# Kernel optimization log

Hardware: AMD Instinct MI355X
Metric: run time of the kernel (lower is better)

## Reference

```python
import jax, jax.numpy as jnp
import numpy as np

IN_FEATURES = 4096
OUT_FEATURES = 11008
GROUP_SIZE = 128
N_HIGH = 1024   # int(0.25*4096)//8*8
N_LOW = 3072    # (4096-1024)//8*8
M_TOKENS = 64


def unpack_6bit(packed, original_k):
    # packed: [K*3//4, N] uint8 values stored as int32
    _, N = packed.shape
    p = packed.reshape(original_k // 4, 3, N)
    b0, b1, b2 = p[:, 0], p[:, 1], p[:, 2]
    v0 = b0 & 63
    v1 = ((b0 >> 6) & 3) | ((b1 & 15) << 2)
    v2 = ((b1 >> 4) & 15) | ((b2 & 3) << 4)
    v3 = (b2 >> 2) & 63
    return jnp.stack([v0, v1, v2, v3], axis=1).reshape(original_k, N)


def unpack_5bit(packed, original_k):
    # packed: [K*5//8, N]
    _, N = packed.shape
    p = packed.reshape(original_k // 8, 5, N)
    b = [p[:, i] for i in range(5)]
    v0 = b[0] & 31
    v1 = ((b[0] >> 5) & 7) | ((b[1] & 3) << 3)
    v2 = (b[1] >> 2) & 31
    v3 = ((b[1] >> 7) & 1) | ((b[2] & 15) << 1)
    v4 = ((b[2] >> 4) & 15) | ((b[3] & 1) << 4)
    v5 = (b[3] >> 1) & 31
    v6 = ((b[3] >> 6) & 3) | ((b[4] & 7) << 2)
    v7 = (b[4] >> 3) & 31
    return jnp.stack([v0, v1, v2, v3, v4, v5, v6, v7], axis=1).reshape(original_k, N)


def dequant_region(W_q, scales, half_range):
    # W_q: [K, N] ints in [0, 2*half_range]; scales: [num_groups, N]
    K, N = W_q.shape
    G = scales.shape[0]
    Wg = (W_q.astype(jnp.float32) - float(half_range)).reshape(G, GROUP_SIZE, N)
    return (Wg * scales[:, None, :]).reshape(K, N)


def setup_inputs() -> dict:
    key = jax.random.key(0)
    ks = jax.random.split(key, 7)
    x = jax.random.normal(ks[0], (M_TOKENS, IN_FEATURES), dtype=jnp.float32)
    W_high_packed = jax.random.randint(ks[1], (N_HIGH * 3 // 4, OUT_FEATURES), 0, 256, dtype=jnp.int32)
    W_low_packed = jax.random.randint(ks[2], (N_LOW * 5 // 8, OUT_FEATURES), 0, 256, dtype=jnp.int32)
    scales_high = jax.random.uniform(ks[3], (N_HIGH // GROUP_SIZE, OUT_FEATURES), dtype=jnp.float32) * 0.02 + 1e-4
    scales_low = jax.random.uniform(ks[4], (N_LOW // GROUP_SIZE, OUT_FEATURES), dtype=jnp.float32) * 0.02 + 1e-4
    col_indices = jax.random.permutation(ks[5], IN_FEATURES).astype(jnp.int32)
    bias = jax.random.normal(ks[6], (OUT_FEATURES,), dtype=jnp.float32) * 0.02
    return {"x": x, "W_high_packed": W_high_packed, "W_low_packed": W_low_packed,
            "scales_high": scales_high, "scales_low": scales_low,
            "col_indices": col_indices, "bias": bias}


def reference(x, W_high_packed, W_low_packed, scales_high, scales_low, col_indices, bias):
    # Unpack mixed 6-bit / 5-bit weights and group-dequantize.
    Wq_high = unpack_6bit(W_high_packed, N_HIGH)          # [1024, N], 0..63
    Wq_low = unpack_5bit(W_low_packed, N_LOW)             # [3072, N], 0..31
    W_high = dequant_region(Wq_high, scales_high, 31)     # 6-bit half_range = 31
    W_low = dequant_region(Wq_low, scales_low, 15)        # 5-bit half_range = 15
    # Column-sensitivity reorder of activations, then split high/low regions.
    x_perm = x[:, col_indices]                            # [M, K]
    x_high = x_perm[:, :N_HIGH]
    x_low = x_perm[:, N_HIGH:N_HIGH + N_LOW]
    out = x_high @ W_high + x_low @ W_low + bias          # [M, N]
    return out
```

## Files before the change

### kernel.cpp

```cpp
#include <hip/hip_runtime.h>


#define NFEAT 11008
#define KTOT  4096

#define C2SIZE 45088768u

typedef _Float16     half8 __attribute__((ext_vector_type(8)));
typedef float        f32x4 __attribute__((ext_vector_type(4)));
typedef unsigned int u32x2 __attribute__((ext_vector_type(2)));
typedef unsigned int u32x4 __attribute__((ext_vector_type(4)));

#define GLOAD16(g, l) __builtin_amdgcn_global_load_lds(                         \
    (const __attribute__((address_space(1))) unsigned int*)(g),                 \
    (__attribute__((address_space(3))) unsigned int*)(l), 16, 0, 0)

#define DEQ8(w, s, mo, bf) do {                                                 \
    bf[0] = (_Float16)fmaf((float)((w)[0]         & 255u), (s), (mo));          \
    bf[1] = (_Float16)fmaf((float)(((w)[0] >>  8) & 255u), (s), (mo));          \
    bf[2] = (_Float16)fmaf((float)(((w)[0] >> 16) & 255u), (s), (mo));          \
    bf[3] = (_Float16)fmaf((float)( (w)[0] >> 24        ), (s), (mo));          \
    bf[4] = (_Float16)fmaf((float)((w)[1]         & 255u), (s), (mo));          \
    bf[5] = (_Float16)fmaf((float)(((w)[1] >>  8) & 255u), (s), (mo));          \
    bf[6] = (_Float16)fmaf((float)(((w)[1] >> 16) & 255u), (s), (mo));          \
    bf[7] = (_Float16)fmaf((float)( (w)[1] >> 24        ), (s), (mo));          \
} while (0)

__global__ __launch_bounds__(256) void prep_xfrag(const float* __restrict__ x,
                                                  const int* __restrict__ col,
                                                  _Float16* __restrict__ xfrag) {
    int idx = blockIdx.x * 256 + threadIdx.x;
    int j  = idx & 7;
    int l  = (idx >> 3) & 63;
    int mt = (idx >> 9) & 3;
    int s  = idx >> 11;
    int k  = s * 32 + ((l >> 4) << 3) + j;
    int m  = mt * 16 + (l & 15);
    xfrag[idx] = (_Float16)x[m * KTOT + col[k]];
}

__global__ __launch_bounds__(256) void compact_w(const int* __restrict__ Wh,
                                                 const int* __restrict__ Wl,
                                                 unsigned char* __restrict__ C2) {
    const int bx  = blockIdx.x;
    const int y   = blockIdx.y;
    const int tid = threadIdx.x;
    __shared__ unsigned char Lb[24][132];

    const bool high = (y < 32);
    const int  s    = high ? y : y - 32;
    const int  nrow = high ? 24 : 20;
    const int* src  = (high ? Wh + (size_t)(24 * s) * NFEAT
                            : Wl + (size_t)(20 * s) * NFEAT) + bx * 128;
    const int nint = nrow * 128;
    for (int i = tid; i < nint; i += 256)
        Lb[i >> 7][i & 127] = (unsigned char)(src[(size_t)(i >> 7) * NFEAT + (i & 127)] & 255);
    __syncthreads();

    const int sg  = high ? s : 32 + s;
    const int L   = (2 * tid) & 63;
    const int gcl = tid >> 5;
    const int o   = L >> 4;

    unsigned int ow[4];
#pragma unroll
    for (int u = 0; u < 2; ++u) {
        const int c = gcl * 16 + ((L + u) & 15);
        unsigned int v0, v1, v2, v3, v4, v5, v6, v7;
        if (high) {
            const unsigned int b0 = Lb[6 * o + 0][c], b1 = Lb[6 * o + 1][c];
            const unsigned int b2 = Lb[6 * o + 2][c], b3 = Lb[6 * o + 3][c];
            const unsigned int b4 = Lb[6 * o + 4][c], b5 = Lb[6 * o + 5][c];
            v0 = b0 & 63;
            v1 = ((b0 >> 6) & 3) | ((b1 & 15) << 2);
            v2 = ((b1 >> 4) & 15) | ((b2 & 3) << 4);
            v3 = (b2 >> 2) & 63;
            v4 = b3 & 63;
            v5 = ((b3 >> 6) & 3) | ((b4 & 15) << 2);
            v6 = ((b4 >> 4) & 15) | ((b5 & 3) << 4);
            v7 = (b5 >> 2) & 63;
        } else {
            const unsigned int b0 = Lb[5 * o + 0][c], b1 = Lb[5 * o + 1][c];
            const unsigned int b2 = Lb[5 * o + 2][c], b3 = Lb[5 * o + 3][c];
            const unsigned int b4 = Lb[5 * o + 4][c];
            v0 = b0 & 31;
            v1 = ((b0 >> 5) & 7) | ((b1 & 3) << 3);
            v2 = (b1 >> 2) & 31;
            v3 = ((b1 >> 7) & 1) | ((b2 & 15) << 1);
            v4 = ((b2 >> 4) & 15) | ((b3 & 1) << 4);
            v5 = (b3 >> 1) & 31;
            v6 = ((b3 >> 6) & 3) | ((b4 & 7) << 2);
            v7 = (b4 >> 3) & 31;
        }
        ow[2 * u]     = v0 | (v1 << 8) | (v2 << 16) | (v3 << 24);
        ow[2 * u + 1] = v4 | (v5 << 8) | (v6 << 16) | (v7 << 24);
    }
    const size_t gc = (size_t)bx * 8 + gcl;
    u32x4* dp = (u32x4*)(C2 + (gc * 128 + sg) * 512 + L * 8);
    *dp = (u32x4){ow[0], ow[1], ow[2], ow[3]};
}

__global__ __launch_bounds__(256, 2) void gemm_kernel(const unsigned char* __restrict__ C2,
                                                      const float* __restrict__ sh,
                                                      const float* __restrict__ sl,
                                                      const _Float16* __restrict__ xfrag,
                                                      float* __restrict__ dst,
                                                      int atomic_mode) {
    const int bx   = blockIdx.x;
    const int kc   = blockIdx.y;
    const int lane = threadIdx.x & 63;
    const int wave = threadIdx.x >> 6;
    const int ci   = lane & 15;
    const int n0   = bx * 128;

    __shared__ __align__(16) _Float16 Ald[32768];

    {
        const char* asrc = (const char*)xfrag + (size_t)kc * 65536;
        const char* ldst = (char*)Ald;
#pragma unroll
        for (int i = 0; i < 16; ++i)
            GLOAD16(asrc + ((size_t)threadIdx.x + i * 256) * 16,
                    ldst + ((size_t)threadIdx.x + i * 256) * 16);
    }

    const bool  high = (kc < 2);
    const float hr   = high ? 31.0f : 15.0f;
    float sc[4][2], mo[4][2];
#pragma unroll
    for (int g = 0; g < 4; ++g)
#pragma unroll
        for (int ng = 0; ng < 2; ++ng) {
            const int n = n0 + wave * 32 + ng * 16 + ci;
            const float s = high ? sh[(size_t)(kc * 4 + g) * NFEAT + n]
                                 : sl[(size_t)((kc - 2) * 4 + g) * NFEAT + n];
            sc[g][ng] = s;
            mo[g][ng] = -hr * s;
        }

    const size_t gc0 = (size_t)bx * 8 + wave * 2;
    const unsigned char* bW0 = C2 + ((gc0 + 0) * 128 + kc * 16) * 512 + lane * 8;
    const unsigned char* bW1 = C2 + ((gc0 + 1) * 128 + kc * 16) * 512 + lane * 8;

    f32x4 acc[4][2];
#pragma unroll
    for (int i = 0; i < 4; ++i)
#pragma unroll
        for (int j = 0; j < 2; ++j) acc[i][j] = (f32x4){0.f, 0.f, 0.f, 0.f};

    __syncthreads();

#pragma unroll
    for (int t = 0; t < 16; ++t) {
        const u32x2 w0 = *(const u32x2*)(bW0 + t * 512);
        const u32x2 w1 = *(const u32x2*)(bW1 + t * 512);
        const int g = t >> 2;
        half8 b0, b1;
        DEQ8(w0, sc[g][0], mo[g][0], b0);
        DEQ8(w1, sc[g][1], mo[g][1], b1);
#pragma unroll
        for (int mt = 0; mt < 4; ++mt) {
            half8 a = *(const half8*)&Ald[((t * 4 + mt) * 64 + lane) * 8];
            acc[mt][0] = __builtin_amdgcn_mfma_f32_16x16x32_f16(a, b0, acc[mt][0], 0, 0, 0);
            acc[mt][1] = __builtin_amdgcn_mfma_f32_16x16x32_f16(a, b1, acc[mt][1], 0, 0, 0);
        }
    }

    const int r0 = (lane >> 4) << 2;
    if (atomic_mode) {
#pragma unroll
        for (int mt = 0; mt < 4; ++mt)
#pragma unroll
            for (int ng = 0; ng < 2; ++ng)
#pragma unroll
                for (int r = 0; r < 4; ++r)
                    atomicAdd(&dst[(size_t)(mt * 16 + r0 + r) * NFEAT + n0 + wave * 32 + ng * 16 + ci],
                              acc[mt][ng][r]);
    } else {
        float* base = dst + (size_t)kc * 64 * NFEAT;
#pragma unroll
        for (int mt = 0; mt < 4; ++mt)
#pragma unroll
            for (int ng = 0; ng < 2; ++ng)
#pragma unroll
                for (int r = 0; r < 4; ++r)
                    base[(size_t)(mt * 16 + r0 + r) * NFEAT + n0 + wave * 32 + ng * 16 + ci] = acc[mt][ng][r];
    }
}

__global__ __launch_bounds__(256, 4) void gemm_direct(const int* __restrict__ Wh,
                                                      const int* __restrict__ Wl,
                                                      const float* __restrict__ sh,
                                                      const float* __restrict__ sl,
                                                      const _Float16* __restrict__ xfrag,
                                                      float* __restrict__ dst) {
    const int n0   = blockIdx.x * 64;
    const int kc   = blockIdx.y;
    const int k0   = kc * 512;
    const int lane = threadIdx.x & 63;
    const int wave = threadIdx.x >> 6;
    const int n  = n0 + wave * 16 + (lane & 15);
    const int kb = (lane >> 4) << 3;

    f32x4 acc[4];
#pragma unroll
    for (int i = 0; i < 4; ++i) acc[i] = (f32x4){0.f, 0.f, 0.f, 0.f};

    if (k0 < 1024) {
        for (int g = 0; g < 4; ++g) {
            const float s    = sh[((k0 >> 7) + g) * NFEAT + n];
            const float moff = -31.0f * s;
#pragma unroll
            for (int st = 0; st < 4; ++st) {
                const int k = k0 + g * 128 + st * 32 + kb;
                const int* bp = Wh + 3 * (k >> 2) * NFEAT + n;
                const int b0 = bp[0];         const int b1 = bp[NFEAT];
                const int b2 = bp[2 * NFEAT]; const int b3 = bp[3 * NFEAT];
                const int b4 = bp[4 * NFEAT]; const int b5 = bp[5 * NFEAT];
                int v0 = b0 & 63;
                int v1 = ((b0 >> 6) & 3) | ((b1 & 15) << 2);
                int v2 = ((b1 >> 4) & 15) | ((b2 & 3) << 4);
                int v3 = (b2 >> 2) & 63;
                int v4 = b3 & 63;
                int v5 = ((b3 >> 6) & 3) | ((b4 & 15) << 2);
                int v6 = ((b4 >> 4) & 15) | ((b5 & 3) << 4);
                int v7 = (b5 >> 2) & 63;
                half8 b;
                b[0] = (_Float16)fmaf((float)v0, s, moff);
                b[1] = (_Float16)fmaf((float)v1, s, moff);
                b[2] = (_Float16)fmaf((float)v2, s, moff);
                b[3] = (_Float16)fmaf((float)v3, s, moff);
                b[4] = (_Float16)fmaf((float)v4, s, moff);
                b[5] = (_Float16)fmaf((float)v5, s, moff);
                b[6] = (_Float16)fmaf((float)v6, s, moff);
                b[7] = (_Float16)fmaf((float)v7, s, moff);
                const int sg = (k0 >> 5) + g * 4 + st;
#pragma unroll
                for (int mt = 0; mt < 4; ++mt) {
                    half8 a = *(const half8*)(xfrag + (((sg * 4 + mt) * 64 + lane) << 3));
                    acc[mt] = __builtin_amdgcn_mfma_f32_16x16x32_f16(a, b, acc[mt], 0, 0, 0);
                }
            }
        }
    } else {
        const int kl0 = k0 - 1024;
        for (int g = 0; g < 4; ++g) {
            const float s    = sl[((kl0 >> 7) + g) * NFEAT + n];
            const float moff = -15.0f * s;
#pragma unroll
            for (int st = 0; st < 4; ++st) {
                const int kl = kl0 + g * 128 + st * 32 + kb;
                const int* bp = Wl + 5 * (kl >> 3) * NFEAT + n;
                const int b0 = bp[0];         const int b1 = bp[NFEAT];
                const int b2 = bp[2 * NFEAT]; const int b3 = bp[3 * NFEAT];
                const int b4 = bp[4 * NFEAT];
                int v0 = b0 & 31;
                int v1 = ((b0 >> 5) & 7) | ((b1 & 3) << 3);
                int v2 = (b1 >> 2) & 31;
                int v3 = ((b1 >> 7) & 1) | ((b2 & 15) << 1);
                int v4 = ((b2 >> 4) & 15) | ((b3 & 1) << 4);
                int v5 = (b3 >> 1) & 31;
                int v6 = ((b3 >> 6) & 3) | ((b4 & 7) << 2);
                int v7 = (b4 >> 3) & 31;
                half8 b;
                b[0] = (_Float16)fmaf((float)v0, s, moff);
                b[1] = (_Float16)fmaf((float)v1, s, moff);
                b[2] = (_Float16)fmaf((float)v2, s, moff);
                b[3] = (_Float16)fmaf((float)v3, s, moff);
                b[4] = (_Float16)fmaf((float)v4, s, moff);
                b[5] = (_Float16)fmaf((float)v5, s, moff);
                b[6] = (_Float16)fmaf((float)v6, s, moff);
                b[7] = (_Float16)fmaf((float)v7, s, moff);
                const int sg = 32 + (kl0 >> 5) + g * 4 + st;
#pragma unroll
                for (int mt = 0; mt < 4; ++mt) {
                    half8 a = *(const half8*)(xfrag + (((sg * 4 + mt) * 64 + lane) << 3));
                    acc[mt] = __builtin_amdgcn_mfma_f32_16x16x32_f16(a, b, acc[mt], 0, 0, 0);
                }
            }
        }
    }

    const int r0 = (lane >> 4) << 2;
#pragma unroll
    for (int mt = 0; mt < 4; ++mt)
#pragma unroll
        for (int r = 0; r < 4; ++r)
            atomicAdd(&dst[(mt * 16 + r0 + r) * NFEAT + n], acc[mt][r]);
}

__global__ __launch_bounds__(256) void reduce_out(const float* __restrict__ part,
                                                  const float* __restrict__ bias,
                                                  float* __restrict__ out, int nc) {
    const int idx = blockIdx.x * 256 + threadIdx.x;
    const int f   = idx * 4;
    const int n   = f % NFEAT;
    f32x4 sum = *(const f32x4*)(bias + n);
    for (int c = 0; c < nc; ++c)
        sum += *(const f32x4*)(part + (size_t)c * 704512 + f);
    *(f32x4*)(out + f) = sum;
}

__global__ __launch_bounds__(256) void init_bias(const float* __restrict__ bias,
                                                 float* __restrict__ out) {
    const int idx = blockIdx.x * 256 + threadIdx.x;
    out[idx] = bias[idx % NFEAT];
}

extern "C" void kernel_launch(void* const* d_in, const int* in_sizes, int n_in,
                              void* d_out, int out_size, void* d_ws, size_t ws_size,
                              hipStream_t stream) {
    const float* x    = (const float*)d_in[0];
    const int*   Wh   = (const int*)d_in[1];
    const int*   Wl   = (const int*)d_in[2];
    const float* sh   = (const float*)d_in[3];
    const float* sl   = (const float*)d_in[4];
    const int*   col  = (const int*)d_in[5];
    const float* bias = (const float*)d_in[6];
    float* out = (float*)d_out;

    _Float16* xfrag = (_Float16*)d_ws;
    const size_t xo = 524288;
    const size_t part_bytes = 8ull * 64 * NFEAT * sizeof(float);

    prep_xfrag<<<1024, 256, 0, stream>>>(x, col, xfrag);

    if (ws_size >= xo + part_bytes + C2SIZE) {
        float*         part = (float*)((char*)d_ws + xo);
        unsigned char* C2   = (unsigned char*)d_ws + xo + part_bytes;
        compact_w<<<dim3(86, 128), 256, 0, stream>>>(Wh, Wl, C2);
        gemm_kernel<<<dim3(86, 8), 256, 0, stream>>>(C2, sh, sl, xfrag, part, 0);
        reduce_out<<<688, 256, 0, stream>>>(part, bias, out, 8);
    } else if (ws_size >= xo + C2SIZE) {
        unsigned char* C2 = (unsigned char*)d_ws + xo;
        compact_w<<<dim3(86, 128), 256, 0, stream>>>(Wh, Wl, C2);
        init_bias<<<2752, 256, 0, stream>>>(bias, out);
        gemm_kernel<<<dim3(86, 8), 256, 0, stream>>>(C2, sh, sl, xfrag, out, 1);
    } else {
        init_bias<<<2752, 256, 0, stream>>>(bias, out);
        gemm_direct<<<dim3(172, 8), 256, 0, stream>>>(Wh, Wl, sh, sl, xfrag, out);
    }
}
```

Measured before the change: 203.6 us.

## Split weight compaction into coalesced strip and transpose passes; drop LDS staging in GEMM

New measurement: 201.0 us. Within noise of the previous version (-1.3%).

```diff
diff --git a/kernel.cpp b/kernel.cpp
--- a/kernel.cpp
+++ b/kernel.cpp
@@ -4,16 +4,14 @@
 #define NFEAT 11008
 #define KTOT  4096
 
-#define C2SIZE 45088768u
+#define WBH_BYTES 8454144u
+#define WB_BYTES  29589504u
+#define C3_BYTES  45088768u
 
 typedef _Float16     half8 __attribute__((ext_vector_type(8)));
 typedef float        f32x4 __attribute__((ext_vector_type(4)));
 typedef unsigned int u32x2 __attribute__((ext_vector_type(2)));
 typedef unsigned int u32x4 __attribute__((ext_vector_type(4)));
-
-#define GLOAD16(g, l) __builtin_amdgcn_global_load_lds(                         \
-    (const __attribute__((address_space(1))) unsigned int*)(g),                 \
-    (__attribute__((address_space(3))) unsigned int*)(l), 16, 0, 0)
 
 #define DEQ8(w, s, mo, bf) do {                                                 \
     bf[0] = (_Float16)fmaf((float)((w)[0]         & 255u), (s), (mo));          \
@@ -39,22 +37,35 @@
     xfrag[idx] = (_Float16)x[m * KTOT + col[k]];
 }
 
-__global__ __launch_bounds__(256) void compact_w(const int* __restrict__ Wh,
+__global__ __launch_bounds__(256) void strip_low(const int* __restrict__ Wh,
                                                  const int* __restrict__ Wl,
-                                                 unsigned char* __restrict__ C2) {
+                                                 unsigned int* __restrict__ WB4) {
+    const unsigned int u = blockIdx.x * 256 + threadIdx.x;
+    const int* s = (u < 2113536u) ? Wh + (size_t)u * 4
+                                  : Wl + ((size_t)u - 2113536u) * 4;
+    u32x4 v = *(const u32x4*)s;
+    WB4[u] = (v[0] & 255u) | ((v[1] & 255u) << 8) |
+             ((v[2] & 255u) << 16) | ((v[3] & 255u) << 24);
+}
+
+__global__ __launch_bounds__(256) void transpose_w(const unsigned char* __restrict__ WB,
+                                                   unsigned char* __restrict__ C3) {
     const int bx  = blockIdx.x;
     const int y   = blockIdx.y;
     const int tid = threadIdx.x;
-    __shared__ unsigned char Lb[24][132];
+    __shared__ __align__(16) unsigned char Lbyte[24 * 144];
 
     const bool high = (y < 32);
     const int  s    = high ? y : y - 32;
     const int  nrow = high ? 24 : 20;
-    const int* src  = (high ? Wh + (size_t)(24 * s) * NFEAT
-                            : Wl + (size_t)(20 * s) * NFEAT) + bx * 128;
-    const int nint = nrow * 128;
-    for (int i = tid; i < nint; i += 256)
-        Lb[i >> 7][i & 127] = (unsigned char)(src[(size_t)(i >> 7) * NFEAT + (i & 127)] & 255);
+    const unsigned char* src = WB + (high ? 0u : WBH_BYTES)
+                             + (size_t)(nrow * s) * NFEAT + bx * 128;
+    const int nchunk = nrow * 8;
+    if (tid < nchunk) {
+        const int row = tid >> 3, ch = tid & 7;
+        *(u32x4*)&Lbyte[row * 144 + ch * 16] =
+            *(const u32x4*)(src + (size_t)row * NFEAT + ch * 16);
+    }
     __syncthreads();
 
     const int sg  = high ? s : 32 + s;
@@ -68,9 +79,12 @@
         const int c = gcl * 16 + ((L + u) & 15);
         unsigned int v0, v1, v2, v3, v4, v5, v6, v7;
         if (high) {
-            const unsigned int b0 = Lb[6 * o + 0][c], b1 = Lb[6 * o + 1][c];
-            const unsigned int b2 = Lb[6 * o + 2][c], b3 = Lb[6 * o + 3][c];
-            const unsigned int b4 = Lb[6 * o + 4][c], b5 = Lb[6 * o + 5][c];
+            const unsigned int b0 = Lbyte[(6 * o + 0) * 144 + c];
+            const unsigned int b1 = Lbyte[(6 * o + 1) * 144 + c];
+            const unsigned int b2 = Lbyte[(6 * o + 2) * 144 + c];
+            const unsigned int b3 = Lbyte[(6 * o + 3) * 144 + c];
+            const unsigned int b4 = Lbyte[(6 * o + 4) * 144 + c];
+            const unsigned int b5 = Lbyte[(6 * o + 5) * 144 + c];
             v0 = b0 & 63;
             v1 = ((b0 >> 6) & 3) | ((b1 & 15) << 2);
             v2 = ((b1 >> 4) & 15) | ((b2 & 3) << 4);
@@ -80,9 +94,11 @@
             v6 = ((b4 >> 4) & 15) | ((b5 & 3) << 4);
             v7 = (b5 >> 2) & 63;
         } else {
-            const unsigned int b0 = Lb[5 * o + 0][c], b1 = Lb[5 * o + 1][c];
-            const unsigned int b2 = Lb[5 * o + 2][c], b3 = Lb[5 * o + 3][c];
-            const unsigned int b4 = Lb[5 * o + 4][c];
+            const unsigned int b0 = Lbyte[(5 * o + 0) * 144 + c];
+            const unsigned int b1 = Lbyte[(5 * o + 1) * 144 + c];
+            const unsigned int b2 = Lbyte[(5 * o + 2) * 144 + c];
+            const unsigned int b3 = Lbyte[(5 * o + 3) * 144 + c];
+            const unsigned int b4 = Lbyte[(5 * o + 4) * 144 + c];
             v0 = b0 & 31;
             v1 = ((b0 >> 5) & 7) | ((b1 & 3) << 3);
             v2 = (b1 >> 2) & 31;
@@ -95,12 +111,14 @@
         ow[2 * u]     = v0 | (v1 << 8) | (v2 << 16) | (v3 << 24);
         ow[2 * u + 1] = v4 | (v5 << 8) | (v6 << 16) | (v7 << 24);
     }
-    const size_t gc = (size_t)bx * 8 + gcl;
-    u32x4* dp = (u32x4*)(C2 + (gc * 128 + sg) * 512 + L * 8);
+    const int w = gcl >> 1, half = gcl & 1;
+    const int kc = sg >> 4, t = sg & 15;
+    u32x4* dp = (u32x4*)(C3 + ((((size_t)bx * 4 + w) * 8 + kc) * 16 + t) * 1024
+                            + half * 512 + L * 8);
     *dp = (u32x4){ow[0], ow[1], ow[2], ow[3]};
 }
 
-__global__ __launch_bounds__(256, 2) void gemm_kernel(const unsigned char* __restrict__ C2,
+__global__ __launch_bounds__(256, 4) void gemm_kernel(const unsigned char* __restrict__ C3,
                                                       const float* __restrict__ sh,
                                                       const float* __restrict__ sl,
                                                       const _Float16* __restrict__ xfrag,
@@ -113,17 +131,6 @@
     const int ci   = lane & 15;
     const int n0   = bx * 128;
 
-    __shared__ __align__(16) _Float16 Ald[32768];
-
-    {
-        const char* asrc = (const char*)xfrag + (size_t)kc * 65536;
-        const char* ldst = (char*)Ald;
-#pragma unroll
-        for (int i = 0; i < 16; ++i)
-            GLOAD16(asrc + ((size_t)threadIdx.x + i * 256) * 16,
-                    ldst + ((size_t)threadIdx.x + i * 256) * 16);
-    }
-
     const bool  high = (kc < 2);
     const float hr   = high ? 31.0f : 15.0f;
     float sc[4][2], mo[4][2];
@@ -138,9 +145,7 @@
             mo[g][ng] = -hr * s;
         }
 
-    const size_t gc0 = (size_t)bx * 8 + wave * 2;
-    const unsigned char* bW0 = C2 + ((gc0 + 0) * 128 + kc * 16) * 512 + lane * 8;
-    const unsigned char* bW1 = C2 + ((gc0 + 1) * 128 + kc * 16) * 512 + lane * 8;
+    const unsigned char* pw = C3 + ((((size_t)bx * 4 + wave) * 8 + kc) << 14) + lane * 8;
 
     f32x4 acc[4][2];
 #pragma unroll
@@ -148,19 +153,18 @@
 #pragma unroll
         for (int j = 0; j < 2; ++j) acc[i][j] = (f32x4){0.f, 0.f, 0.f, 0.f};
 
-    __syncthreads();
-
 #pragma unroll
     for (int t = 0; t < 16; ++t) {
-        const u32x2 w0 = *(const u32x2*)(bW0 + t * 512);
-        const u32x2 w1 = *(const u32x2*)(bW1 + t * 512);
+        const u32x2 w0 = *(const u32x2*)(pw + t * 1024);
+        const u32x2 w1 = *(const u32x2*)(pw + t * 1024 + 512);
         const int g = t >> 2;
         half8 b0, b1;
         DEQ8(w0, sc[g][0], mo[g][0], b0);
         DEQ8(w1, sc[g][1], mo[g][1], b1);
 #pragma unroll
         for (int mt = 0; mt < 4; ++mt) {
-            half8 a = *(const half8*)&Ald[((t * 4 + mt) * 64 + lane) * 8];
+            half8 a = *(const half8*)(xfrag +
+                (((size_t)((kc * 16 + t) * 4 + mt) * 64 + lane) << 3));
             acc[mt][0] = __builtin_amdgcn_mfma_f32_16x16x32_f16(a, b0, acc[mt][0], 0, 0, 0);
             acc[mt][1] = __builtin_amdgcn_mfma_f32_16x16x32_f16(a, b1, acc[mt][1], 0, 0, 0);
         }
@@ -320,22 +324,26 @@
     float* out = (float*)d_out;
 
     _Float16* xfrag = (_Float16*)d_ws;
-    const size_t xo = 524288;
+    const size_t xo         = 524288;
     const size_t part_bytes = 8ull * 64 * NFEAT * sizeof(float);
 
     prep_xfrag<<<1024, 256, 0, stream>>>(x, col, xfrag);
 
-    if (ws_size >= xo + part_bytes + C2SIZE) {
+    if (ws_size >= xo + part_bytes + WB_BYTES + C3_BYTES) {
         float*         part = (float*)((char*)d_ws + xo);
-        unsigned char* C2   = (unsigned char*)d_ws + xo + part_bytes;
-        compact_w<<<dim3(86, 128), 256, 0, stream>>>(Wh, Wl, C2);
-        gemm_kernel<<<dim3(86, 8), 256, 0, stream>>>(C2, sh, sl, xfrag, part, 0);
+        unsigned char* WB   = (unsigned char*)d_ws + xo + part_bytes;
+        unsigned char* C3   = WB + WB_BYTES;
+        strip_low<<<28896, 256, 0, stream>>>(Wh, Wl, (unsigned int*)WB);
+        transpose_w<<<dim3(86, 128), 256, 0, stream>>>(WB, C3);
+        gemm_kernel<<<dim3(86, 8), 256, 0, stream>>>(C3, sh, sl, xfrag, part, 0);
         reduce_out<<<688, 256, 0, stream>>>(part, bias, out, 8);
-    } else if (ws_size >= xo + C2SIZE) {
-        unsigned char* C2 = (unsigned char*)d_ws + xo;
-        compact_w<<<dim3(86, 128), 256, 0, stream>>>(Wh, Wl, C2);
+    } else if (ws_size >= xo + WB_BYTES + C3_BYTES) {
+        unsigned char* WB = (unsigned char*)d_ws + xo;
+        unsigned char* C3 = WB + WB_BYTES;
+        strip_low<<<28896, 256, 0, stream>>>(Wh, Wl, (unsigned int*)WB);
+        transpose_w<<<dim3(86, 128), 256, 0, stream>>>(WB, C3);
         init_bias<<<2752, 256, 0, stream>>>(bias, out);
-        gemm_kernel<<<dim3(86, 8), 256, 0, stream>>>(C2, sh, sl, xfrag, out, 1);
+        gemm_kernel<<<dim3(86, 8), 256, 0, stream>>>(C3, sh, sl, xfrag, out, 1);
     } else {
         init_bias<<<2752, 256, 0, stream>>>(bias, out);
         gemm_direct<<<dim3(172, 8), 256, 0, stream>>>(Wh, Wl, sh, sl, xfrag, out);
```
